# Performance work log

Hardware: AMD Instinct MI355X
Metric: run time of the kernel (lower is better)

Reference implementation:

```python
import jax, jax.numpy as jnp
import numpy as np

N_NODES = 10000
N_EDGES = 160000
NUM_FEAT = 14
DIM = 256


def gat_conv(x, src, dst, W, a_s, a_d, b, concat):
    """PyG GATConv: W [H*C, F_in], a_s/a_d [H, C], edges src->dst (self-loops included)."""
    H, C = a_s.shape
    N = x.shape[0]
    h = (x @ W.T).reshape(N, H, C)                       # [N,H,C]
    alpha_src = (h * a_s).sum(-1)                        # [N,H]
    alpha_dst = (h * a_d).sum(-1)                        # [N,H]
    e = jax.nn.leaky_relu(alpha_src[src] + alpha_dst[dst], negative_slope=0.2)  # [E,H]
    emax = jax.ops.segment_max(e, dst, num_segments=N)   # [N,H]
    emax = jnp.where(jnp.isneginf(emax), 0.0, emax)
    ex = jnp.exp(e - emax[dst])
    denom = jax.ops.segment_sum(ex, dst, num_segments=N)
    coef = ex / (denom[dst] + 1e-16)                     # segment softmax over in-edges
    out = jax.ops.segment_sum(h[src] * coef[..., None], dst, num_segments=N)  # [N,H,C]
    out = out.reshape(N, H * C) if concat else out.mean(axis=1)
    return out + b


def setup_inputs() -> dict:
    key = jax.random.key(0)
    ks = jax.random.split(key, 24)
    d = DIM
    f = NUM_FEAT
    def w(k, shape, fan_in):
        return jax.random.normal(k, shape, dtype=jnp.float32) * (1.0 / np.sqrt(fan_in))
    inp = {
        "x": jax.random.normal(ks[0], (N_NODES, f), dtype=jnp.float32),
        "edge_index": jax.random.randint(ks[1], (2, N_EDGES), 0, N_NODES, dtype=jnp.int64
                                         if jax.config.jax_enable_x64 else jnp.int32),
        # conv1: 14 -> 4 heads x 256
        "W1": w(ks[2], (4 * d, f), f),
        "a1s": w(ks[3], (4, d), d), "a1d": w(ks[4], (4, d), d),
        "b1": jnp.zeros((4 * d,), jnp.float32),
        "lw1": w(ks[5], (4 * d, f), f), "lb1": jnp.zeros((4 * d,), jnp.float32),
        # conv2: 1024 -> 4 heads x 256
        "W2": w(ks[6], (4 * d, 4 * d), 4 * d),
        "a2s": w(ks[7], (4, d), d), "a2d": w(ks[8], (4, d), d),
        "b2": jnp.zeros((4 * d,), jnp.float32),
        "lw2": w(ks[9], (4 * d, 4 * d), 4 * d), "lb2": jnp.zeros((4 * d,), jnp.float32),
        # conv3: 1024 -> 6 heads x 256, mean over heads
        "W3": w(ks[10], (6 * d, 4 * d), 4 * d),
        "a3s": w(ks[11], (6, d), d), "a3d": w(ks[12], (6, d), d),
        "b3": jnp.zeros((d,), jnp.float32),
        "lw3": w(ks[13], (d, 4 * d), 4 * d), "lb3": jnp.zeros((d,), jnp.float32),
    }
    return inp


def reference(x, edge_index, W1, a1s, a1d, b1, lw1, lb1,
              W2, a2s, a2d, b2, lw2, lb2,
              W3, a3s, a3d, b3, lw3, lb3):
    N = x.shape[0]
    loops = jnp.arange(N, dtype=edge_index.dtype)
    src = jnp.concatenate([edge_index[0], loops])
    dst = jnp.concatenate([edge_index[1], loops])
    x1 = jax.nn.elu(gat_conv(x, src, dst, W1, a1s, a1d, b1, True) + x @ lw1.T + lb1)
    x2 = jax.nn.elu(gat_conv(x1, src, dst, W2, a2s, a2d, b2, True) + x1 @ lw2.T + lb2)
    x3 = gat_conv(x2, src, dst, W3, a3s, a3d, b3, False) + x2 @ lw3.T + lb3
    return x3
```

## Files before the change

### kernel.cpp

```cpp
#include <hip/hip_runtime.h>
#include <hip/hip_bf16.h>
#include <cstddef>

#define NN 10000
#define EE0 160000
#define NF 14
#define DC 256

static inline int ceildiv(int a, int b) { return (a + b - 1) / b; }

__device__ __forceinline__ float lrelu02(float x) { return fmaxf(x, 0.2f * x); }

__device__ __forceinline__ short f2bf(float f) {
    unsigned u = __float_as_uint(f);
    unsigned r = (u + 0x7FFFu + ((u >> 16) & 1u)) >> 16;
    return (short)r;
}
__device__ __forceinline__ float bf2f(short s) {
    return __uint_as_float(((unsigned)(unsigned short)s) << 16);
}

typedef __attribute__((ext_vector_type(8))) short bf16x8;
typedef __attribute__((ext_vector_type(4))) float f32x4;

#define GLDS(gaddr, laddr)                                                         \
    __builtin_amdgcn_global_load_lds(                                              \
        (__attribute__((address_space(1))) void*)(gaddr),                          \
        (__attribute__((address_space(3))) void*)(laddr), 16, 0, 0)

__global__ void count_edges_k(const int* __restrict__ ei, int* __restrict__ counts,
                              int E0, int N) {
    int e = blockIdx.x * 256 + threadIdx.x;
    int E = E0 + N;
    if (e >= E) return;
    int dst = (e < E0) ? ei[E0 + e] : (e - E0);
    atomicAdd(&counts[dst], 1);
}

__global__ __launch_bounds__(1024) void scan_k(const int* __restrict__ counts,
                                               int* __restrict__ row_off, int n) {
    __shared__ int sums[1024];
    int t = threadIdx.x;
    int chunk = (n + 1023) >> 10;
    int base = t * chunk;
    int lim = base + chunk; if (lim > n) lim = n;
    int s = 0;
    for (int i = base; i < lim; ++i) s += counts[i];
    sums[t] = s;
    __syncthreads();
    for (int off = 1; off < 1024; off <<= 1) {
        int v = (t >= off) ? sums[t - off] : 0;
        __syncthreads();
        sums[t] += v;
        __syncthreads();
    }
    int run = (t == 0) ? 0 : sums[t - 1];
    for (int i = base; i < lim; ++i) { run += counts[i]; row_off[i + 1] = run; }
    if (t == 0) row_off[0] = 0;
}

__global__ void scatter_k(const int* __restrict__ ei, const int* __restrict__ row_off,
                          int* __restrict__ cursor, int* __restrict__ csr_src,
                          int E0, int N) {
    int e = blockIdx.x * 256 + threadIdx.x;
    int E = E0 + N;
    if (e >= E) return;
    int src, dst;
    if (e < E0) { src = ei[e]; dst = ei[E0 + e]; }
    else        { src = dst = e - E0; }
    int pos = row_off[dst] + atomicAdd(&cursor[dst], 1);
    csr_src[pos] = src;
}

__global__ __launch_bounds__(256) void cvt_bf16_fused_k(
    const float* __restrict__ p0, short* __restrict__ q0, int n0,
    const float* __restrict__ p1, short* __restrict__ q1, int n1,
    const float* __restrict__ p2, short* __restrict__ q2, int n2,
    const float* __restrict__ p3, short* __restrict__ q3, int n3) {
    int i = blockIdx.x * 256 + threadIdx.x;
    const float* in; short* out; int idx;
    if (i < n0) { in = p0; out = q0; idx = i; }
    else if (i < n0 + n1) { in = p1; out = q1; idx = i - n0; }
    else if (i < n0 + n1 + n2) { in = p2; out = q2; idx = i - n0 - n1; }
    else if (i < n0 + n1 + n2 + n3) { in = p3; out = q3; idx = i - n0 - n1 - n2; }
    else return;
    float4 v = ((const float4*)in)[idx];
    short4 o;
    o.x = f2bf(v.x); o.y = f2bf(v.y); o.z = f2bf(v.z); o.w = f2bf(v.w);
    ((short4*)out)[idx] = o;
}

__global__ __launch_bounds__(256) void pad_bf16_k(
    const float* __restrict__ p0, short* __restrict__ q0, int r0,
    const float* __restrict__ p1, short* __restrict__ q1, int r1,
    const float* __restrict__ p2, short* __restrict__ q2, int r2,
    int K, int Kp) {
    int i = blockIdx.x * 256 + threadIdx.x;
    int rows = r0 + r1 + r2;
    int total = rows * Kp;
    if (i >= total) return;
    int row = i / Kp, col = i - row * Kp;
    const float* in; short* out; int r;
    if (row < r0) { in = p0; out = q0; r = row; }
    else if (row < r0 + r1) { in = p1; out = q1; r = row - r0; }
    else { in = p2; out = q2; r = row - r0 - r1; }
    out[(size_t)r * Kp + col] = (col < K) ? f2bf(in[(size_t)r * K + col]) : (short)0;
}

__global__ __launch_bounds__(256) void gemm_bf16_dual(
    const short* __restrict__ A, const short* __restrict__ B,
    const float* __restrict__ b1, const float* __restrict__ b2,
    const float* __restrict__ a_s, const float* __restrict__ a_d,
    float* __restrict__ ps, float* __restrict__ pd,
    short* __restrict__ Cb, void* __restrict__ Cf, int lin_bf16,
    int M, int Nh, int Nf, int K, int H) {
    __shared__ short As[128 * 32];
    __shared__ short Bs[128 * 32];
    const int t = threadIdx.x;
    const int wave = t >> 6, lane = t & 63;
    const int m0 = blockIdx.y * 128, n0 = blockIdx.x * 128;
    const int wm = (wave >> 1) * 64, wn = (wave & 1) * 64;
    const int lane15 = lane & 15, quad = lane >> 4;

    const int lrow = lane >> 2;
    const int lk = ((lane & 3) ^ ((lrow >> 1) & 3)) * 8;
    int arow0 = m0 + wave * 16 + lrow;
    int arow1 = arow0 + 64;
    if (arow0 > M - 1) arow0 = M - 1;
    if (arow1 > M - 1) arow1 = M - 1;
    const short* ag0 = A + (size_t)arow0 * K + lk;
    const short* ag1 = A + (size_t)arow1 * K + lk;
    const short* bg0 = B + (size_t)(n0 + wave * 16 + lrow) * K + lk;
    const short* bg1 = B + (size_t)(n0 + 64 + wave * 16 + lrow) * K + lk;
    short* al0 = &As[(wave * 16) * 32];
    short* al1 = &As[(64 + wave * 16) * 32];
    short* bl0 = &Bs[(wave * 16) * 32];
    short* bl1 = &Bs[(64 + wave * 16) * 32];

    const int rql = (quad ^ ((lane15 >> 1) & 3)) * 8;

    f32x4 acc[4][4];
#pragma unroll
    for (int i = 0; i < 4; ++i)
#pragma unroll
        for (int j = 0; j < 4; ++j) acc[i][j] = (f32x4){0.f, 0.f, 0.f, 0.f};

    for (int k0 = 0; k0 < K; k0 += 32) {
        GLDS(ag0 + k0, al0);
        GLDS(ag1 + k0, al1);
        GLDS(bg0 + k0, bl0);
        GLDS(bg1 + k0, bl1);
        __syncthreads();
        bf16x8 af[4], bfr[4];
#pragma unroll
        for (int i = 0; i < 4; ++i)
            af[i] = *(const bf16x8*)&As[(wm + 16 * i + lane15) * 32 + rql];
#pragma unroll
        for (int j = 0; j < 4; ++j)
            bfr[j] = *(const bf16x8*)&Bs[(wn + 16 * j + lane15) * 32 + rql];
#pragma unroll
        for (int i = 0; i < 4; ++i)
#pragma unroll
            for (int j = 0; j < 4; ++j)
                acc[i][j] = __builtin_amdgcn_mfma_f32_16x16x32_bf16(
                    af[i], bfr[j], acc[i][j], 0, 0, 0);
        __syncthreads();
    }

    if (n0 >= Nh) {
#pragma unroll
        for (int j = 0; j < 4; ++j) {
            int nc = n0 - Nh + wn + 16 * j + lane15;
            float bias = b1[nc] + b2[nc];
#pragma unroll
            for (int i = 0; i < 4; ++i) {
                int mb = m0 + wm + 16 * i + quad * 4;
#pragma unroll
                for (int r = 0; r < 4; ++r) {
                    int m = mb + r;
                    if (m < M) {
                        float v = acc[i][j][r] + bias;
                        if (lin_bf16) ((short*)Cf)[(size_t)m * Nf + nc] = f2bf(v);
                        else          ((float*)Cf)[(size_t)m * Nf + nc] = v;
                    }
                }
            }
        }
    } else {
        const int chunk = (n0 + wn) >> 6;
        const int head = chunk >> 2;
        const int cb = (n0 + wn) & 255;
        float asv[4], adv[4];
#pragma unroll
        for (int j = 0; j < 4; ++j) {
            asv[j] = a_s[head * DC + cb + 16 * j + lane15];
            adv[j] = a_d[head * DC + cb + 16 * j + lane15];
        }
#pragma unroll
        for (int j = 0; j < 4; ++j) {
            int n = n0 + wn + 16 * j + lane15;
#pragma unroll
            for (int i = 0; i < 4; ++i) {
                int mb = m0 + wm + 16 * i + quad * 4;
#pragma unroll
                for (int r = 0; r < 4; ++r) {
                    int m = mb + r;
                    if (m < M) Cb[(size_t)m * Nh + n] = f2bf(acc[i][j][r]);
                }
            }
        }
        float* psc = ps + (size_t)chunk * M;
        float* pdc = pd + (size_t)chunk * M;
#pragma unroll
        for (int i = 0; i < 4; ++i) {
#pragma unroll
            for (int r = 0; r < 4; ++r) {
                float s = acc[i][0][r] * asv[0] + acc[i][1][r] * asv[1] +
                          acc[i][2][r] * asv[2] + acc[i][3][r] * asv[3];
                float d = acc[i][0][r] * adv[0] + acc[i][1][r] * adv[1] +
                          acc[i][2][r] * adv[2] + acc[i][3][r] * adv[3];
#pragma unroll
                for (int off = 8; off > 0; off >>= 1) {
                    s += __shfl_xor(s, off);
                    d += __shfl_xor(d, off);
                }
                int m = m0 + wm + 16 * i + quad * 4 + r;
                if (lane15 == 0 && m < M) { psc[m] = s; pdc[m] = d; }
            }
        }
    }
}

__global__ __launch_bounds__(256) void alpha_reduce_k(
    const float* __restrict__ ps, const float* __restrict__ pd,
    float* __restrict__ asrc, float* __restrict__ adst, int M, int H) {
    int m = blockIdx.x * 256 + threadIdx.x;
    int h = blockIdx.y;
    if (m >= M) return;
    float s = 0.f, d = 0.f;
#pragma unroll
    for (int c = 0; c < 4; ++c) {
        s += ps[(size_t)(h * 4 + c) * M + m];
        d += pd[(size_t)(h * 4 + c) * M + m];
    }
    asrc[m * H + h] = s;
    adst[m * H + h] = d;
}

__global__ __launch_bounds__(256) void gat_agg(
    const short* __restrict__ hbuf, const short* __restrict__ lin,
    const float* __restrict__ asrc, const float* __restrict__ adst_a,
    const int* __restrict__ row_off, const int* __restrict__ csr_src,
    short* __restrict__ outx, int N, int H) {
    int wid = (int)((blockIdx.x * (size_t)blockDim.x + threadIdx.x) >> 6);
    int lane = threadIdx.x & 63;
    if (wid >= N * H) return;
    int n = wid / H, hh = wid - n * H;
    int beg = row_off[n], end = row_off[n + 1];
    int deg = end - beg;
    float ad = adst_a[wid];

    size_t cbase = (size_t)n * H * DC + hh * DC + lane * 4;
    const short4 lv = *(const short4*)(lin + cbase);
    float4 acc = make_float4(bf2f(lv.x), bf2f(lv.y), bf2f(lv.z), bf2f(lv.w));

    if (deg <= 64) {
        int s = 0; float e = -1e38f;
        if (lane < deg) {
            s = csr_src[beg + lane];
            e = lrelu02(asrc[s * H + hh] + ad);
        }
        float m = e;
#pragma unroll
        for (int off = 32; off > 0; off >>= 1) m = fmaxf(m, __shfl_xor(m, off));
        float p = (lane < deg) ? __expf(e - m) : 0.f;
        float dsum = p;
#pragma unroll
        for (int off = 32; off > 0; off >>= 1) dsum += __shfl_xor(dsum, off);
        float coef = p / (dsum + 1e-16f);

        const size_t hoff = (size_t)hh * DC + lane * 4;
        int i = 0;
        for (; i + 8 <= deg; i += 8) {
            short4 v[8]; float wv[8];
#pragma unroll
            for (int u = 0; u < 8; ++u) {
                int su = __shfl(s, i + u);
                v[u] = *(const short4*)(hbuf + (size_t)su * (H * DC) + hoff);
                wv[u] = __shfl(coef, i + u);
            }
#pragma unroll
            for (int u = 0; u < 8; ++u) {
                acc.x += wv[u] * bf2f(v[u].x);
                acc.y += wv[u] * bf2f(v[u].y);
                acc.z += wv[u] * bf2f(v[u].z);
                acc.w += wv[u] * bf2f(v[u].w);
            }
        }
        for (; i < deg; ++i) {
            float wv = __shfl(coef, i);
            int si = __shfl(s, i);
            const short4 hv = *(const short4*)(hbuf + (size_t)si * (H * DC) + hoff);
            acc.x += wv * bf2f(hv.x); acc.y += wv * bf2f(hv.y);
            acc.z += wv * bf2f(hv.z); acc.w += wv * bf2f(hv.w);
        }
    } else {
        float m = -1e38f;
        for (int i = beg + lane; i < end; i += 64) {
            int s = csr_src[i];
            m = fmaxf(m, lrelu02(asrc[s * H + hh] + ad));
        }
#pragma unroll
        for (int off = 32; off > 0; off >>= 1) m = fmaxf(m, __shfl_xor(m, off));
        float dsum = 0.f;
        for (int i = beg + lane; i < end; i += 64) {
            int s = csr_src[i];
            dsum += __expf(lrelu02(asrc[s * H + hh] + ad) - m);
        }
#pragma unroll
        for (int off = 32; off > 0; off >>= 1) dsum += __shfl_xor(dsum, off);
        float inv = 1.f / (dsum + 1e-16f);
        for (int i = beg; i < end; ++i) {
            int s = csr_src[i];
            float wv = __expf(lrelu02(asrc[s * H + hh] + ad) - m) * inv;
            const short4 hv = *(const short4*)(hbuf + ((size_t)s * H + hh) * DC + lane * 4);
            acc.x += wv * bf2f(hv.x); acc.y += wv * bf2f(hv.y);
            acc.z += wv * bf2f(hv.z); acc.w += wv * bf2f(hv.w);
        }
    }
    acc.x = acc.x > 0.f ? acc.x : __expf(acc.x) - 1.f;
    acc.y = acc.y > 0.f ? acc.y : __expf(acc.y) - 1.f;
    acc.z = acc.z > 0.f ? acc.z : __expf(acc.z) - 1.f;
    acc.w = acc.w > 0.f ? acc.w : __expf(acc.w) - 1.f;
    short4 o;
    o.x = f2bf(acc.x); o.y = f2bf(acc.y); o.z = f2bf(acc.z); o.w = f2bf(acc.w);
    *(short4*)(outx + cbase) = o;
}

__global__ __launch_bounds__(384) void gat_agg_mean(
    const short* __restrict__ hbuf, const float* __restrict__ asrc,
    const float* __restrict__ adst_a, const int* __restrict__ row_off,
    const int* __restrict__ csr_src, float* __restrict__ out, int N) {
    const int H = 6;
    __shared__ float red[6][DC];
    int n = blockIdx.x;
    int wave = threadIdx.x >> 6, lane = threadIdx.x & 63;
    int hh = wave;
    int beg = row_off[n], end = row_off[n + 1];
    int deg = end - beg;
    const float invH = 1.f / 6.f;
    float ad = adst_a[n * H + hh];

    float4 acc = make_float4(0.f, 0.f, 0.f, 0.f);
    const size_t hoff = (size_t)hh * DC + lane * 4;

    if (deg <= 64) {
        int s = 0; float e = -1e38f;
        if (lane < deg) {
            s = csr_src[beg + lane];
            e = lrelu02(asrc[s * H + hh] + ad);
        }
        float m = e;
#pragma unroll
        for (int off = 32; off > 0; off >>= 1) m = fmaxf(m, __shfl_xor(m, off));
        float p = (lane < deg) ? __expf(e - m) : 0.f;
        float dsum = p;
#pragma unroll
        for (int off = 32; off > 0; off >>= 1) dsum += __shfl_xor(dsum, off);
        float coef = p * invH / (dsum + 1e-16f);

        int i = 0;
        for (; i + 8 <= deg; i += 8) {
            short4 v[8]; float wv[8];
#pragma unroll
            for (int u = 0; u < 8; ++u) {
                int su = __shfl(s, i + u);
                v[u] = *(const short4*)(hbuf + (size_t)su * (H * DC) + hoff);
                wv[u] = __shfl(coef, i + u);
            }
#pragma unroll
            for (int u = 0; u < 8; ++u) {
                acc.x += wv[u] * bf2f(v[u].x);
                acc.y += wv[u] * bf2f(v[u].y);
                acc.z += wv[u] * bf2f(v[u].z);
                acc.w += wv[u] * bf2f(v[u].w);
            }
        }
        for (; i < deg; ++i) {
            float wv = __shfl(coef, i);
            int si = __shfl(s, i);
            const short4 hv = *(const short4*)(hbuf + (size_t)si * (H * DC) + hoff);
            acc.x += wv * bf2f(hv.x); acc.y += wv * bf2f(hv.y);
            acc.z += wv * bf2f(hv.z); acc.w += wv * bf2f(hv.w);
        }
    } else {
        float m = -1e38f;
        for (int i = beg + lane; i < end; i += 64) {
            int s = csr_src[i];
            m = fmaxf(m, lrelu02(asrc[s * H + hh] + ad));
        }
#pragma unroll
        for (int off = 32; off > 0; off >>= 1) m = fmaxf(m, __shfl_xor(m, off));
        float dsum = 0.f;
        for (int i = beg + lane; i < end; i += 64) {
            int s = csr_src[i];
            dsum += __expf(lrelu02(asrc[s * H + hh] + ad) - m);
        }
#pragma unroll
        for (int off = 32; off > 0; off >>= 1) dsum += __shfl_xor(dsum, off);
        float inv = invH / (dsum + 1e-16f);
        for (int i = beg; i < end; ++i) {
            int s = csr_src[i];
            float wv = __expf(lrelu02(asrc[s * H + hh] + ad) - m) * inv;
            const short4 hv = *(const short4*)(hbuf + (size_t)s * (H * DC) + hoff);
            acc.x += wv * bf2f(hv.x); acc.y += wv * bf2f(hv.y);
            acc.z += wv * bf2f(hv.z); acc.w += wv * bf2f(hv.w);
        }
    }
    *(float4*)&red[wave][lane * 4] = acc;
    __syncthreads();
    if (wave == 0) {
        float* op = out + (size_t)n * DC + lane * 4;
        float4 o = *(float4*)op;
#pragma unroll
        for (int j = 0; j < 6; ++j) {
            float4 r = *(float4*)&red[j][lane * 4];
            o.x += r.x; o.y += r.y; o.z += r.z; o.w += r.w;
        }
        *(float4*)op = o;
    }
}

extern "C" void kernel_launch(void* const* d_in, const int* in_sizes, int n_in,
                              void* d_out, int out_size, void* d_ws, size_t ws_size,
                              hipStream_t stream) {
    const float* x   = (const float*)d_in[0];
    const int*   ei  = (const int*)d_in[1];
    const float* W1  = (const float*)d_in[2];
    const float* a1s = (const float*)d_in[3];
    const float* a1d = (const float*)d_in[4];
    const float* b1  = (const float*)d_in[5];
    const float* lw1 = (const float*)d_in[6];
    const float* lb1 = (const float*)d_in[7];
    const float* W2  = (const float*)d_in[8];
    const float* a2s = (const float*)d_in[9];
    const float* a2d = (const float*)d_in[10];
    const float* b2  = (const float*)d_in[11];
    const float* lb2_w = (const float*)d_in[12];
    const float* lb2 = (const float*)d_in[13];
    const float* W3  = (const float*)d_in[14];
    const float* a3s = (const float*)d_in[15];
    const float* a3d = (const float*)d_in[16];
    const float* b3  = (const float*)d_in[17];
    const float* lw3 = (const float*)d_in[18];
    const float* lb3 = (const float*)d_in[19];
    const float* lw2 = lb2_w;
    float* out = (float*)d_out;

    const int N = NN, E0 = EE0, E = EE0 + NN;

    unsigned char* w = (unsigned char*)d_ws;
    size_t off = 0;
    auto alloc = [&](size_t bytes) {
        void* p = w + off;
        off += (bytes + 255) & ~(size_t)255;
        return p;
    };
    short* hbuf   = (short*)alloc((size_t)N * 1536 * 2);
    short* buf    = (short*)alloc((size_t)N * 1024 * 2);
    short* xb     = (short*)alloc((size_t)N * 1024 * 2);
    short* xpad   = (short*)alloc((size_t)N * 32 * 2);
    short* W1p    = (short*)alloc((size_t)1024 * 32 * 2);
    short* lw1p   = (short*)alloc((size_t)1024 * 32 * 2);
    short* W2b    = (short*)alloc((size_t)1024 * 1024 * 2);
    short* lw2b   = (short*)alloc((size_t)1024 * 1024 * 2);
    short* W3b    = (short*)alloc((size_t)1536 * 1024 * 2);
    short* lw3b   = (short*)alloc((size_t)256 * 1024 * 2);
    float* psrc   = (float*)alloc((size_t)24 * N * 4);
    float* pdst   = (float*)alloc((size_t)24 * N * 4);
    float* asrc   = (float*)alloc((size_t)N * 6 * 4);
    float* adst   = (float*)alloc((size_t)N * 6 * 4);
    int* row_off  = (int*)alloc((size_t)(N + 1) * 4);
    int* counts2  = (int*)alloc((size_t)2 * N * 4);
    int* counts   = counts2;
    int* cursor   = counts2 + N;
    int* csr_src  = (int*)alloc((size_t)E * 4);
    (void)ws_size; (void)n_in; (void)in_sizes; (void)out_size;

    hipMemsetAsync(counts2, 0, (size_t)2 * N * 4, stream);
    count_edges_k<<<ceildiv(E, 256), 256, 0, stream>>>(ei, counts, E0, N);
    scan_k<<<1, 1024, 0, stream>>>(counts, row_off, N);
    scatter_k<<<ceildiv(E, 256), 256, 0, stream>>>(ei, row_off, cursor, csr_src, E0, N);

    {
        int q0 = 1024 * 1024 / 4, q1 = 1024 * 1024 / 4, q2 = 1536 * 1024 / 4,
            q3 = 256 * 1024 / 4;
        cvt_bf16_fused_k<<<ceildiv(q0 + q1 + q2 + q3, 256), 256, 0, stream>>>(
            W2, W2b, q0, lw2, lw2b, q1, W3, W3b, q2, lw3, lw3b, q3);
        int rows = N + 1024 + 1024;
        pad_bf16_k<<<ceildiv(rows * 32, 256), 256, 0, stream>>>(
            x, xpad, N, W1, W1p, 1024, lw1, lw1p, 1024, NF, 32);
    }

    gemm_bf16_dual<<<dim3(16, ceildiv(N, 128)), 256, 0, stream>>>(
        xpad, W1p, b1, lb1, a1s, a1d, psrc, pdst, hbuf, (void*)buf, 1,
        N, 1024, 1024, 32, 4);
    alpha_reduce_k<<<dim3(ceildiv(N, 256), 4), 256, 0, stream>>>(
        psrc, pdst, asrc, adst, N, 4);
    gat_agg<<<ceildiv(N * 4, 4), 256, 0, stream>>>(hbuf, buf, asrc, adst, row_off,
                                                   csr_src, xb, N, 4);

    gemm_bf16_dual<<<dim3(16, ceildiv(N, 128)), 256, 0, stream>>>(
        xb, W2b, b2, lb2, a2s, a2d, psrc, pdst, hbuf, (void*)buf, 1,
        N, 1024, 1024, 1024, 4);
    alpha_reduce_k<<<dim3(ceildiv(N, 256), 4), 256, 0, stream>>>(
        psrc, pdst, asrc, adst, N, 4);
    gat_agg<<<ceildiv(N * 4, 4), 256, 0, stream>>>(hbuf, buf, asrc, adst, row_off,
                                                   csr_src, xb, N, 4);

    gemm_bf16_dual<<<dim3(14, ceildiv(N, 128)), 256, 0, stream>>>(
        xb, W3b, b3, lb3, a3s, a3d, psrc, pdst, hbuf, (void*)out, 0,
        N, 1536, 256, 1024, 6);
    alpha_reduce_k<<<dim3(ceildiv(N, 256), 6), 256, 0, stream>>>(
        psrc, pdst, asrc, adst, N, 6);
    gat_agg_mean<<<N, 384, 0, stream>>>(hbuf, asrc, adst, row_off, csr_src, out, N);
}
```

Measured before the change: 472.6 us.

## Process two heads per wave in GAT aggregation and double K-step in GEMM

The aggregation kernels now let each wave handle a pair of heads. Each lane loads 8 bf16 channels with 16-byte gathers instead of 4 with 8-byte loads, and both heads' attention logits come from one float2 load, which halves the number of waves and row-index/softmax passes per node. The GEMM main loop now stages two 32-wide K slices into separate LDS buffers before each barrier, halving the barrier count at the cost of twice the LDS. The wider per-lane accumulators raise register pressure, and the mean kernel drops to 192 threads per block.

```diff
diff --git a/kernel.cpp b/kernel.cpp
--- a/kernel.cpp
+++ b/kernel.cpp
@@ -114,8 +114,8 @@
     float* __restrict__ ps, float* __restrict__ pd,
     short* __restrict__ Cb, void* __restrict__ Cf, int lin_bf16,
     int M, int Nh, int Nf, int K, int H) {
-    __shared__ short As[128 * 32];
-    __shared__ short Bs[128 * 32];
+    __shared__ short As[2][128 * 32];
+    __shared__ short Bs[2][128 * 32];
     const int t = threadIdx.x;
     const int wave = t >> 6, lane = t & 63;
     const int m0 = blockIdx.y * 128, n0 = blockIdx.x * 128;
@@ -132,10 +132,8 @@
     const short* ag1 = A + (size_t)arow1 * K + lk;
     const short* bg0 = B + (size_t)(n0 + wave * 16 + lrow) * K + lk;
     const short* bg1 = B + (size_t)(n0 + 64 + wave * 16 + lrow) * K + lk;
-    short* al0 = &As[(wave * 16) * 32];
-    short* al1 = &As[(64 + wave * 16) * 32];
-    short* bl0 = &Bs[(wave * 16) * 32];
-    short* bl1 = &Bs[(64 + wave * 16) * 32];
+    const int alo0 = (wave * 16) * 32;
+    const int alo1 = (64 + wave * 16) * 32;
 
     const int rql = (quad ^ ((lane15 >> 1) & 3)) * 8;
 
@@ -145,25 +143,49 @@
 #pragma unroll
         for (int j = 0; j < 4; ++j) acc[i][j] = (f32x4){0.f, 0.f, 0.f, 0.f};
 
-    for (int k0 = 0; k0 < K; k0 += 32) {
-        GLDS(ag0 + k0, al0);
-        GLDS(ag1 + k0, al1);
-        GLDS(bg0 + k0, bl0);
-        GLDS(bg1 + k0, bl1);
+    for (int k0 = 0; k0 < K; k0 += 64) {
+        GLDS(ag0 + k0, &As[0][alo0]);
+        GLDS(ag1 + k0, &As[0][alo1]);
+        GLDS(bg0 + k0, &Bs[0][alo0]);
+        GLDS(bg1 + k0, &Bs[0][alo1]);
+        const bool two = (k0 + 32 < K);
+        if (two) {
+            GLDS(ag0 + k0 + 32, &As[1][alo0]);
+            GLDS(ag1 + k0 + 32, &As[1][alo1]);
+            GLDS(bg0 + k0 + 32, &Bs[1][alo0]);
+            GLDS(bg1 + k0 + 32, &Bs[1][alo1]);
+        }
         __syncthreads();
-        bf16x8 af[4], bfr[4];
-#pragma unroll
-        for (int i = 0; i < 4; ++i)
-            af[i] = *(const bf16x8*)&As[(wm + 16 * i + lane15) * 32 + rql];
-#pragma unroll
-        for (int j = 0; j < 4; ++j)
-            bfr[j] = *(const bf16x8*)&Bs[(wn + 16 * j + lane15) * 32 + rql];
-#pragma unroll
-        for (int i = 0; i < 4; ++i)
+        {
+            bf16x8 af[4], bfr[4];
+#pragma unroll
+            for (int i = 0; i < 4; ++i)
+                af[i] = *(const bf16x8*)&As[0][(wm + 16 * i + lane15) * 32 + rql];
 #pragma unroll
             for (int j = 0; j < 4; ++j)
-                acc[i][j] = __builtin_amdgcn_mfma_f32_16x16x32_bf16(
-                    af[i], bfr[j], acc[i][j], 0, 0, 0);
+                bfr[j] = *(const bf16x8*)&Bs[0][(wn + 16 * j + lane15) * 32 + rql];
+#pragma unroll
+            for (int i = 0; i < 4; ++i)
+#pragma unroll
+                for (int j = 0; j < 4; ++j)
+                    acc[i][j] = __builtin_amdgcn_mfma_f32_16x16x32_bf16(
+                        af[i], bfr[j], acc[i][j], 0, 0, 0);
+        }
+        if (two) {
+            bf16x8 af[4], bfr[4];
+#pragma unroll
+            for (int i = 0; i < 4; ++i)
+                af[i] = *(const bf16x8*)&As[1][(wm + 16 * i + lane15) * 32 + rql];
+#pragma unroll
+            for (int j = 0; j < 4; ++j)
+                bfr[j] = *(const bf16x8*)&Bs[1][(wn + 16 * j + lane15) * 32 + rql];
+#pragma unroll
+            for (int i = 0; i < 4; ++i)
+#pragma unroll
+                for (int j = 0; j < 4; ++j)
+                    acc[i][j] = __builtin_amdgcn_mfma_f32_16x16x32_bf16(
+                        af[i], bfr[j], acc[i][j], 0, 0, 0);
+        }
         __syncthreads();
     }
 
@@ -254,90 +276,123 @@
     short* __restrict__ outx, int N, int H) {
     int wid = (int)((blockIdx.x * (size_t)blockDim.x + threadIdx.x) >> 6);
     int lane = threadIdx.x & 63;
-    if (wid >= N * H) return;
-    int n = wid / H, hh = wid - n * H;
+    int HP = H >> 1;
+    if (wid >= N * HP) return;
+    int n = wid / HP, hp = wid - n * HP;
+    int hA = hp * 2;
     int beg = row_off[n], end = row_off[n + 1];
     int deg = end - beg;
-    float ad = adst_a[wid];
-
-    size_t cbase = (size_t)n * H * DC + hh * DC + lane * 4;
-    const short4 lv = *(const short4*)(lin + cbase);
-    float4 acc = make_float4(bf2f(lv.x), bf2f(lv.y), bf2f(lv.z), bf2f(lv.w));
+    const float2 adp = *(const float2*)(adst_a + (size_t)n * H + hA);
+    const bool loH = (lane < 32);
+
+    size_t cbase = (size_t)n * (H * DC) + (size_t)hA * DC + lane * 8;
+    float acc[8];
+    {
+        bf16x8 lv = *(const bf16x8*)(lin + cbase);
+#pragma unroll
+        for (int j = 0; j < 8; ++j) acc[j] = bf2f(lv[j]);
+    }
+    const size_t hoff = (size_t)hA * DC + lane * 8;
 
     if (deg <= 64) {
-        int s = 0; float e = -1e38f;
+        int s = 0; float eA = -1e38f, eB = -1e38f;
         if (lane < deg) {
             s = csr_src[beg + lane];
-            e = lrelu02(asrc[s * H + hh] + ad);
-        }
-        float m = e;
-#pragma unroll
-        for (int off = 32; off > 0; off >>= 1) m = fmaxf(m, __shfl_xor(m, off));
-        float p = (lane < deg) ? __expf(e - m) : 0.f;
-        float dsum = p;
-#pragma unroll
-        for (int off = 32; off > 0; off >>= 1) dsum += __shfl_xor(dsum, off);
-        float coef = p / (dsum + 1e-16f);
-
-        const size_t hoff = (size_t)hh * DC + lane * 4;
+            float2 av = *(const float2*)(asrc + (size_t)s * H + hA);
+            eA = lrelu02(av.x + adp.x);
+            eB = lrelu02(av.y + adp.y);
+        }
+        float mA = eA, mB = eB;
+#pragma unroll
+        for (int off = 32; off > 0; off >>= 1) {
+            mA = fmaxf(mA, __shfl_xor(mA, off));
+            mB = fmaxf(mB, __shfl_xor(mB, off));
+        }
+        float pA = (lane < deg) ? __expf(eA - mA) : 0.f;
+        float pB = (lane < deg) ? __expf(eB - mB) : 0.f;
+        float sA = pA, sB = pB;
+#pragma unroll
+        for (int off = 32; off > 0; off >>= 1) {
+            sA += __shfl_xor(sA, off);
+            sB += __shfl_xor(sB, off);
+        }
+        float coefA = pA / (sA + 1e-16f);
+        float coefB = pB / (sB + 1e-16f);
+
         int i = 0;
         for (; i + 8 <= deg; i += 8) {
-            short4 v[8]; float wv[8];
+            bf16x8 v[8]; float w[8];
 #pragma unroll
             for (int u = 0; u < 8; ++u) {
                 int su = __shfl(s, i + u);
-                v[u] = *(const short4*)(hbuf + (size_t)su * (H * DC) + hoff);
-                wv[u] = __shfl(coef, i + u);
+                v[u] = *(const bf16x8*)(hbuf + (size_t)su * (H * DC) + hoff);
+                float wA = __shfl(coefA, i + u);
+                float wB = __shfl(coefB, i + u);
+                w[u] = loH ? wA : wB;
             }
 #pragma unroll
-            for (int u = 0; u < 8; ++u) {
-                acc.x += wv[u] * bf2f(v[u].x);
-                acc.y += wv[u] * bf2f(v[u].y);
-                acc.z += wv[u] * bf2f(v[u].z);
-                acc.w += wv[u] * bf2f(v[u].w);
-            }
+            for (int u = 0; u < 8; ++u)
+#pragma unroll
+                for (int j = 0; j < 8; ++j) acc[j] += w[u] * bf2f(v[u][j]);
         }
         for (; i < deg; ++i) {
-            float wv = __shfl(coef, i);
             int si = __shfl(s, i);
-            const short4 hv = *(const short4*)(hbuf + (size_t)si * (H * DC) + hoff);
-            acc.x += wv * bf2f(hv.x); acc.y += wv * bf2f(hv.y);
-            acc.z += wv * bf2f(hv.z); acc.w += wv * bf2f(hv.w);
+            float wA = __shfl(coefA, i);
+            float wB = __shfl(coefB, i);
+            float wv = loH ? wA : wB;
+            const bf16x8 hv = *(const bf16x8*)(hbuf + (size_t)si * (H * DC) + hoff);
+#pragma unroll
+            for (int j = 0; j < 8; ++j) acc[j] += wv * bf2f(hv[j]);
         }
     } else {
-        float m = -1e38f;
+        float mA = -1e38f, mB = -1e38f;
         for (int i = beg + lane; i < end; i += 64) {
             int s = csr_src[i];
-            m = fmaxf(m, lrelu02(asrc[s * H + hh] + ad));
-        }
-#pragma unroll
-        for (int off = 32; off > 0; off >>= 1) m = fmaxf(m, __shfl_xor(m, off));
-        float dsum = 0.f;
+            float2 av = *(const float2*)(asrc + (size_t)s * H + hA);
+            mA = fmaxf(mA, lrelu02(av.x + adp.x));
+            mB = fmaxf(mB, lrelu02(av.y + adp.y));
+        }
+#pragma unroll
+        for (int off = 32; off > 0; off >>= 1) {
+            mA = fmaxf(mA, __shfl_xor(mA, off));
+            mB = fmaxf(mB, __shfl_xor(mB, off));
+        }
+        float sA = 0.f, sB = 0.f;
         for (int i = beg + lane; i < end; i += 64) {
             int s = csr_src[i];
-            dsum += __expf(lrelu02(asrc[s * H + hh] + ad) - m);
-        }
-#pragma unroll
-        for (int off = 32; off > 0; off >>= 1) dsum += __shfl_xor(dsum, off);
-        float inv = 1.f / (dsum + 1e-16f);
+            float2 av = *(const float2*)(asrc + (size_t)s * H + hA);
+            sA += __expf(lrelu02(av.x + adp.x) - mA);
+            sB += __expf(lrelu02(av.y + adp.y) - mB);
+        }
+#pragma unroll
+        for (int off = 32; off > 0; off >>= 1) {
+            sA += __shfl_xor(sA, off);
+            sB += __shfl_xor(sB, off);
+        }
+        float invA = 1.f / (sA + 1e-16f);
+        float invB = 1.f / (sB + 1e-16f);
         for (int i = beg; i < end; ++i) {
             int s = csr_src[i];
-            float wv = __expf(lrelu02(asrc[s * H + hh] + ad) - m) * inv;
-            const short4 hv = *(const short4*)(hbuf + ((size_t)s * H + hh) * DC + lane * 4);
-            acc.x += wv * bf2f(hv.x); acc.y += wv * bf2f(hv.y);
-            acc.z += wv * bf2f(hv.z); acc.w += wv * bf2f(hv.w);
-        }
-    }
-    acc.x = acc.x > 0.f ? acc.x : __expf(acc.x) - 1.f;
-    acc.y = acc.y > 0.f ? acc.y : __expf(acc.y) - 1.f;
-    acc.z = acc.z > 0.f ? acc.z : __expf(acc.z) - 1.f;
-    acc.w = acc.w > 0.f ? acc.w : __expf(acc.w) - 1.f;
-    short4 o;
-    o.x = f2bf(acc.x); o.y = f2bf(acc.y); o.z = f2bf(acc.z); o.w = f2bf(acc.w);
-    *(short4*)(outx + cbase) = o;
-}
-
-__global__ __launch_bounds__(384) void gat_agg_mean(
+            float2 av = *(const float2*)(asrc + (size_t)s * H + hA);
+            float wA = __expf(lrelu02(av.x + adp.x) - mA) * invA;
+            float wB = __expf(lrelu02(av.y + adp.y) - mB) * invB;
+            float wv = loH ? wA : wB;
+            const bf16x8 hv = *(const bf16x8*)(hbuf + (size_t)s * (H * DC) + hoff);
+#pragma unroll
+            for (int j = 0; j < 8; ++j) acc[j] += wv * bf2f(hv[j]);
+        }
+    }
+    bf16x8 o;
+#pragma unroll
+    for (int j = 0; j < 8; ++j) {
+        float a = acc[j];
+        a = a > 0.f ? a : __expf(a) - 1.f;
+        o[j] = f2bf(a);
+    }
+    *(bf16x8*)(outx + cbase) = o;
+}
+
+__global__ __launch_bounds__(192) void gat_agg_mean(
     const short* __restrict__ hbuf, const float* __restrict__ asrc,
     const float* __restrict__ adst_a, const int* __restrict__ row_off,
     const int* __restrict__ csr_src, float* __restrict__ out, int N) {
@@ -345,79 +400,112 @@
     __shared__ float red[6][DC];
     int n = blockIdx.x;
     int wave = threadIdx.x >> 6, lane = threadIdx.x & 63;
-    int hh = wave;
+    int hA = wave * 2;
     int beg = row_off[n], end = row_off[n + 1];
     int deg = end - beg;
     const float invH = 1.f / 6.f;
-    float ad = adst_a[n * H + hh];
-
-    float4 acc = make_float4(0.f, 0.f, 0.f, 0.f);
-    const size_t hoff = (size_t)hh * DC + lane * 4;
+    const float2 adp = *(const float2*)(adst_a + (size_t)n * H + hA);
+    const bool loH = (lane < 32);
+
+    float acc[8];
+#pragma unroll
+    for (int j = 0; j < 8; ++j) acc[j] = 0.f;
+    const size_t hoff = (size_t)hA * DC + lane * 8;
 
     if (deg <= 64) {
-        int s = 0; float e = -1e38f;
+        int s = 0; float eA = -1e38f, eB = -1e38f;
         if (lane < deg) {
             s = csr_src[beg + lane];
-            e = lrelu02(asrc[s * H + hh] + ad);
-        }
-        float m = e;
-#pragma unroll
-        for (int off = 32; off > 0; off >>= 1) m = fmaxf(m, __shfl_xor(m, off));
-        float p = (lane < deg) ? __expf(e - m) : 0.f;
-        float dsum = p;
-#pragma unroll
-        for (int off = 32; off > 0; off >>= 1) dsum += __shfl_xor(dsum, off);
-        float coef = p * invH / (dsum + 1e-16f);
+            float2 av = *(const float2*)(asrc + (size_t)s * H + hA);
+            eA = lrelu02(av.x + adp.x);
+            eB = lrelu02(av.y + adp.y);
+        }
+        float mA = eA, mB = eB;
+#pragma unroll
+        for (int off = 32; off > 0; off >>= 1) {
+            mA = fmaxf(mA, __shfl_xor(mA, off));
+            mB = fmaxf(mB, __shfl_xor(mB, off));
+        }
+        float pA = (lane < deg) ? __expf(eA - mA) : 0.f;
+        float pB = (lane < deg) ? __expf(eB - mB) : 0.f;
+        float sA = pA, sB = pB;
+#pragma unroll
+        for (int off = 32; off > 0; off >>= 1) {
+            sA += __shfl_xor(sA, off);
+            sB += __shfl_xor(sB, off);
+        }
+        float coefA = pA * invH / (sA + 1e-16f);
+        float coefB = pB * invH / (sB + 1e-16f);
 
         int i = 0;
         for (; i + 8 <= deg; i += 8) {
-            short4 v[8]; float wv[8];
+            bf16x8 v[8]; float w[8];
 #pragma unroll
             for (int u = 0; u < 8; ++u) {
                 int su = __shfl(s, i + u);
-                v[u] = *(const short4*)(hbuf + (size_t)su * (H * DC) + hoff);
-                wv[u] = __shfl(coef, i + u);
+                v[u] = *(const bf16x8*)(hbuf + (size_t)su * (H * DC) + hoff);
+                float wA = __shfl(coefA, i + u);
+                float wB = __shfl(coefB, i + u);
+                w[u] = loH ? wA : wB;
             }
 #pragma unroll
-            for (int u = 0; u < 8; ++u) {
-                acc.x += wv[u] * bf2f(v[u].x);
-                acc.y += wv[u] * bf2f(v[u].y);
-                acc.z += wv[u] * bf2f(v[u].z);
-                acc.w += wv[u] * bf2f(v[u].w);
-            }
+            for (int u = 0; u < 8; ++u)
+#pragma unroll
+                for (int j = 0; j < 8; ++j) acc[j] += w[u] * bf2f(v[u][j]);
         }
         for (; i < deg; ++i) {
-            float wv = __shfl(coef, i);
             int si = __shfl(s, i);
-            const short4 hv = *(const short4*)(hbuf + (size_t)si * (H * DC) + hoff);
-            acc.x += wv * bf2f(hv.x); acc.y += wv * bf2f(hv.y);
-            acc.z += wv * bf2f(hv.z); acc.w += wv * bf2f(hv.w);
+            float wA = __shfl(coefA, i);
+            float wB = __shfl(coefB, i);
+            float wv = loH ? wA : wB;
+            const bf16x8 hv = *(const bf16x8*)(hbuf + (size_t)si * (H * DC) + hoff);
+#pragma unroll
+            for (int j = 0; j < 8; ++j) acc[j] += wv * bf2f(hv[j]);
         }
     } else {
-        float m = -1e38f;
+        float mA = -1e38f, mB = -1e38f;
         for (int i = beg + lane; i < end; i += 64) {
             int s = csr_src[i];
-            m = fmaxf(m, lrelu02(asrc[s * H + hh] + ad));
-        }
-#pragma unroll
-        for (int off = 32; off > 0; off >>= 1) m = fmaxf(m, __shfl_xor(m, off));
-        float dsum = 0.f;
+            float2 av = *(const float2*)(asrc + (size_t)s * H + hA);
+            mA = fmaxf(mA, lrelu02(av.x + adp.x));
+            mB = fmaxf(mB, lrelu02(av.y + adp.y));
+        }
+#pragma unroll
+        for (int off = 32; off > 0; off >>= 1) {
+            mA = fmaxf(mA, __shfl_xor(mA, off));
+            mB = fmaxf(mB, __shfl_xor(mB, off));
+        }
+        float sA = 0.f, sB = 0.f;
         for (int i = beg + lane; i < end; i += 64) {
             int s = csr_src[i];
-            dsum += __expf(lrelu02(asrc[s * H + hh] + ad) - m);
-        }
-#pragma unroll
-        for (int off = 32; off > 0; off >>= 1) dsum += __shfl_xor(dsum, off);
-        float inv = invH / (dsum + 1e-16f);
+            float2 av = *(const float2*)(asrc + (size_t)s * H + hA);
+            sA += __expf(lrelu02(av.x + adp.x) - mA);
+            sB += __expf(lrelu02(av.y + adp.y) - mB);
+        }
+#pragma unroll
+        for (int off = 32; off > 0; off >>= 1) {
+            sA += __shfl_xor(sA, off);
+            sB += __shfl_xor(sB, off);
+        }
+        float invA = invH / (sA + 1e-16f);
+        float invB = invH / (sB + 1e-16f);
         for (int i = beg; i < end; ++i) {
             int s = csr_src[i];
-            float wv = __expf(lrelu02(asrc[s * H + hh] + ad) - m) * inv;
-            const short4 hv = *(const short4*)(hbuf + (size_t)s * (H * DC) + hoff);
-            acc.x += wv * bf2f(hv.x); acc.y += wv * bf2f(hv.y);
-            acc.z += wv * bf2f(hv.z); acc.w += wv * bf2f(hv.w);
-        }
-    }
-    *(float4*)&red[wave][lane * 4] = acc;
+            float2 av = *(const float2*)(asrc + (size_t)s * H + hA);
+            float wA = __expf(lrelu02(av.x + adp.x) - mA) * invA;
+            float wB = __expf(lrelu02(av.y + adp.y) - mB) * invB;
+            float wv = loH ? wA : wB;
+            const bf16x8 hv = *(const bf16x8*)(hbuf + (size_t)s * (H * DC) + hoff);
+#pragma unroll
+            for (int j = 0; j < 8; ++j) acc[j] += wv * bf2f(hv[j]);
+        }
+    }
+    {
+        int head = hA + (loH ? 0 : 1);
+        int ch0 = (lane & 31) * 8;
+        *(float4*)&red[head][ch0]     = make_float4(acc[0], acc[1], acc[2], acc[3]);
+        *(float4*)&red[head][ch0 + 4] = make_float4(acc[4], acc[5], acc[6], acc[7]);
+    }
     __syncthreads();
     if (wave == 0) {
         float* op = out + (size_t)n * DC + lane * 4;
@@ -507,7 +595,7 @@
         N, 1024, 1024, 32, 4);
     alpha_reduce_k<<<dim3(ceildiv(N, 256), 4), 256, 0, stream>>>(
         psrc, pdst, asrc, adst, N, 4);
-    gat_agg<<<ceildiv(N * 4, 4), 256, 0, stream>>>(hbuf, buf, asrc, adst, row_off,
+    gat_agg<<<ceildiv(N * 2, 4), 256, 0, stream>>>(hbuf, buf, asrc, adst, row_off,
                                                    csr_src, xb, N, 4);
 
     gemm_bf16_dual<<<dim3(16, ceildiv(N, 128)), 256, 0, stream>>>(
@@ -515,7 +603,7 @@
         N, 1024, 1024, 1024, 4);
     alpha_reduce_k<<<dim3(ceildiv(N, 256), 4), 256, 0, stream>>>(
         psrc, pdst, asrc, adst, N, 4);
-    gat_agg<<<ceildiv(N * 4, 4), 256, 0, stream>>>(hbuf, buf, asrc, adst, row_off,
+    gat_agg<<<ceildiv(N * 2, 4), 256, 0, stream>>>(hbuf, buf, asrc, adst, row_off,
                                                    csr_src, xb, N, 4);
 
     gemm_bf16_dual<<<dim3(14, ceildiv(N, 128)), 256, 0, stream>>>(
@@ -523,5 +611,5 @@
         N, 1536, 256, 1024, 6);
     alpha_reduce_k<<<dim3(ceildiv(N, 256), 6), 256, 0, stream>>>(
         psrc, pdst, asrc, adst, N, 6);
-    gat_agg_mean<<<N, 384, 0, stream>>>(hbuf, asrc, adst, row_off, csr_src, out, N);
-}
+    gat_agg_mean<<<N, 192, 0, stream>>>(hbuf, asrc, adst, row_off, csr_src, out, N);
+}
```

Measured after the change: 487.3 us. +3.1%, slower.
